# Performance work log

Hardware: AMD Instinct MI355X
Metric: run time of the kernel (lower is better)

## Reference

```python
import jax, jax.numpy as jnp
import numpy as np

N, NX, NQ, NU = 262144, 64, 64, 16
STD = 0.5


def setup_inputs() -> dict:
    key = jax.random.key(0)
    ks = jax.random.split(key, 8)
    x = jax.random.normal(ks[0], (N, NX), jnp.float32)
    u = jax.random.normal(ks[1], (N, NU), jnp.float32)
    A = jax.random.normal(ks[2], (NX, NX), jnp.float32) * STD
    B1 = jax.random.normal(ks[3], (NX, NQ), jnp.float32) * STD
    B2 = jax.random.normal(ks[4], (NX, NU), jnp.float32) * STD
    C1 = jax.random.normal(ks[5], (NQ, NX), jnp.float32) * STD
    # D11 is strictly lower triangular (forward substitution / triangular solve)
    D11 = jnp.tril(jax.random.normal(ks[6], (NQ, NQ), jnp.float32) * STD, -1)
    D12 = jax.random.normal(ks[7], (NQ, NU), jnp.float32) * STD
    bv = jnp.zeros((NQ,), jnp.float32)  # bias=False in original module
    bx = jnp.zeros((NX,), jnp.float32)
    return {"x": x, "u": u, "A": A, "B1": B1, "B2": B2,
            "C1": C1, "D11": D11, "D12": D12, "bv": bv, "bx": bx}


def _calculate_w(x, u, C1, D11, D12, bv):
    """Solve w = act(C1 x + D11 w + D12 u + bv) by forward substitution.
    D11 is strictly lower triangular, so row i of w only depends on rows < i."""
    act = jax.nn.relu
    nq = D11.shape[0]
    base = x @ C1.T + u @ D12.T + bv          # (N, nq): input-dependent part
    eye = jnp.eye(nq, dtype=x.dtype)           # one-hot rows for the scatter

    def step(w, inp):
        d_row, b_col, e = inp                  # (nq,), (N,), (nq,)
        v = b_col + w @ d_row                  # (N,)  uses only already-filled w cols
        w = w + act(v)[:, None] * e            # write column i (matches torch select_w)
        return w, None

    w0 = jnp.zeros((x.shape[0], nq), x.dtype)
    w, _ = jax.lax.scan(step, w0, (D11, base.T, eye))
    return w


def reference(x, u, A, B1, B2, C1, D11, D12, bv, bx):
    # x_dot = A x + B1 w + B2 u + bx
    w = _calculate_w(x, u, C1, D11, D12, bv)
    x_dot = x @ A.T + w @ B1.T + u @ B2.T + bx
    return x_dot
```

## Files before the change

### kernel.cpp

```cpp
#include <hip/hip_runtime.h>
#include <utility>

#define NROWS 262144
#define BT 512
#define RPB 128

typedef float f16v __attribute__((ext_vector_type(16)));


__global__ void prep_kernel(const float* __restrict__ A, const float* __restrict__ B1,
                            const float* __restrict__ B2, const float* __restrict__ C1,
                            const float* __restrict__ D11, const float* __restrict__ D12,
                            const float* __restrict__ bv, const float* __restrict__ bx,
                            float* __restrict__ ws) {
    int g = blockIdx.x * 256 + threadIdx.x;
    if (g < 4096) {
        int r = g >> 6, c = g & 63;
        int to = c * 64 + r;
        ws[0     + to] = C1[g];
        ws[4096  + to] = D11[g];
        ws[9280  + to] = A[g];
        ws[13376 + to] = B1[g];
    }
    if (g < 1024) {
        int r = g >> 4, c = g & 15;
        int to = c * 64 + r;
        ws[8192  + to] = D12[g];
        ws[17472 + to] = B2[g];
    }
    if (g < 64) {
        ws[9216  + g] = bv[g];
        ws[18496 + g] = bx[g];
    }
}

__device__ __forceinline__ f16v lds16(const float* p) { return *(const f16v*)p; }

template<int Q>
__device__ __forceinline__ float qbcast(float v) {
    return __int_as_float(__builtin_amdgcn_update_dpp(
        0, __float_as_int(v), Q * 0x55, 0xF, 0xF, true));
}

template<int I>
__device__ __forceinline__ void substep(f16v& s, const float* D11s, int c16, int c) {
    const float wv = fmaxf(qbcast<(I >> 4)>(s[I & 15]), 0.0f);
    s += lds16(D11s + I * 64 + c16) * wv;
    s[I & 15] = (c == (I >> 4)) ? wv : s[I & 15];
}

template<int... Is>
__device__ __forceinline__ void subst_all(f16v& s, const float* D11s, int c16, int c,
                                          std::integer_sequence<int, Is...>) {
    (substep<Is>(s, D11s, c16, c), ...);
}

template<int J>
__device__ __forceinline__ void b1step(f16v& acc, const f16v& w, const float* B1s, int c16) {
    acc += lds16(B1s + J * 64 + c16) * qbcast<(J >> 4)>(w[J & 15]);
}

template<int... Js>
__device__ __forceinline__ void b1_all(f16v& acc, const f16v& w, const float* B1s, int c16,
                                       std::integer_sequence<int, Js...>) {
    (b1step<Js>(acc, w, B1s, c16), ...);
}

__global__ __launch_bounds__(BT, 4) void renl2_fused(const float* __restrict__ x,
                                                     const float* __restrict__ u,
                                                     const float* __restrict__ ws,
                                                     float* __restrict__ out) {
    __shared__ float sm[9280];
    const int tid = threadIdx.x;
    const int c   = tid & 3;
    const int c16 = c << 4;
    const int r   = tid >> 2;
    const int row = blockIdx.x * RPB + r;

    const float* __restrict__ xr = x + (size_t)row * 64;
    const float* __restrict__ ur = u + (size_t)row * 16;

#pragma unroll 4
    for (int i = tid; i < 9280; i += BT) sm[i] = ws[i];
    __syncthreads();

    f16v s = lds16(sm + 9216 + c16);
#pragma unroll 1
    for (int j = 0; j < 64; j += 4) {
        const float4 xv = *(const float4*)(xr + j);
#pragma unroll
        for (int jj = 0; jj < 4; jj++) {
            const float xs = (jj == 0) ? xv.x : (jj == 1) ? xv.y : (jj == 2) ? xv.z : xv.w;
            s += lds16(sm + (j + jj) * 64 + c16) * xs;
        }
    }
    {
        const float4 uv0 = *(const float4*)(ur);
        const float4 uv1 = *(const float4*)(ur + 4);
        const float4 uv2 = *(const float4*)(ur + 8);
        const float4 uv3 = *(const float4*)(ur + 12);
        const float us[16] = {uv0.x,uv0.y,uv0.z,uv0.w, uv1.x,uv1.y,uv1.z,uv1.w,
                              uv2.x,uv2.y,uv2.z,uv2.w, uv3.x,uv3.y,uv3.z,uv3.w};
#pragma unroll
        for (int j = 0; j < 16; j++)
            s += lds16(sm + 8192 + j * 64 + c16) * us[j];
    }

    subst_all(s, sm + 4096, c16, c, std::make_integer_sequence<int, 64>{});

    __syncthreads();
#pragma unroll 4
    for (int i = tid; i < 9280; i += BT) sm[i] = ws[9280 + i];
    __syncthreads();

    f16v acc = lds16(sm + 9216 + c16);
    b1_all(acc, s, sm + 4096, c16, std::make_integer_sequence<int, 64>{});

#pragma unroll 1
    for (int j = 0; j < 64; j += 4) {
        const float4 xv = *(const float4*)(xr + j);
#pragma unroll
        for (int jj = 0; jj < 4; jj++) {
            const float xs = (jj == 0) ? xv.x : (jj == 1) ? xv.y : (jj == 2) ? xv.z : xv.w;
            acc += lds16(sm + (j + jj) * 64 + c16) * xs;
        }
    }

    {
        const float4 uv0 = *(const float4*)(ur);
        const float4 uv1 = *(const float4*)(ur + 4);
        const float4 uv2 = *(const float4*)(ur + 8);
        const float4 uv3 = *(const float4*)(ur + 12);
        const float us[16] = {uv0.x,uv0.y,uv0.z,uv0.w, uv1.x,uv1.y,uv1.z,uv1.w,
                              uv2.x,uv2.y,uv2.z,uv2.w, uv3.x,uv3.y,uv3.z,uv3.w};
#pragma unroll
        for (int j = 0; j < 16; j++)
            acc += lds16(sm + 8192 + j * 64 + c16) * us[j];
    }

    float* outr = out + (size_t)row * 64;
    *(float4*)(outr + c16)      = float4{acc[0],  acc[1],  acc[2],  acc[3]};
    *(float4*)(outr + c16 + 4)  = float4{acc[4],  acc[5],  acc[6],  acc[7]};
    *(float4*)(outr + c16 + 8)  = float4{acc[8],  acc[9],  acc[10], acc[11]};
    *(float4*)(outr + c16 + 12) = float4{acc[12], acc[13], acc[14], acc[15]};
}

extern "C" void kernel_launch(void* const* d_in, const int* in_sizes, int n_in,
                              void* d_out, int out_size, void* d_ws, size_t ws_size,
                              hipStream_t stream) {
    const float* x   = (const float*)d_in[0];
    const float* u   = (const float*)d_in[1];
    const float* A   = (const float*)d_in[2];
    const float* B1  = (const float*)d_in[3];
    const float* B2  = (const float*)d_in[4];
    const float* C1  = (const float*)d_in[5];
    const float* D11 = (const float*)d_in[6];
    const float* D12 = (const float*)d_in[7];
    const float* bv  = (const float*)d_in[8];
    const float* bx  = (const float*)d_in[9];
    float* out = (float*)d_out;
    float* ws  = (float*)d_ws;

    prep_kernel<<<16, 256, 0, stream>>>(A, B1, B2, C1, D11, D12, bv, bx, ws);
    renl2_fused<<<NROWS / RPB, BT, 0, stream>>>(x, u, ws, out);
}
```

Baseline: 270.0 us.

## Load x/u once into registers, share via DPP, stage all weights in LDS once

```diff
diff --git a/kernel.cpp b/kernel.cpp
--- a/kernel.cpp
+++ b/kernel.cpp
@@ -6,6 +6,7 @@
 #define RPB 128
 
 typedef float f16v __attribute__((ext_vector_type(16)));
+typedef float f4v  __attribute__((ext_vector_type(4)));
 
 
 __global__ void prep_kernel(const float* __restrict__ A, const float* __restrict__ B1,
@@ -56,93 +57,57 @@
 }
 
 template<int J>
-__device__ __forceinline__ void b1step(f16v& acc, const f16v& w, const float* B1s, int c16) {
-    acc += lds16(B1s + J * 64 + c16) * qbcast<(J >> 4)>(w[J & 15]);
+__device__ __forceinline__ void mv64step(f16v& a, const float* Ms, int c16, const f16v& f) {
+    a += lds16(Ms + J * 64 + c16) * qbcast<(J >> 4)>(f[J & 15]);
+}
+template<int... Js>
+__device__ __forceinline__ void mv64(f16v& a, const float* Ms, int c16, const f16v& f,
+                                     std::integer_sequence<int, Js...>) {
+    (mv64step<Js>(a, Ms, c16, f), ...);
 }
 
+template<int J>
+__device__ __forceinline__ void mv16step(f16v& a, const float* Ms, int c16, const f4v& f) {
+    a += lds16(Ms + J * 64 + c16) * qbcast<(J >> 2)>(f[J & 3]);
+}
 template<int... Js>
-__device__ __forceinline__ void b1_all(f16v& acc, const f16v& w, const float* B1s, int c16,
-                                       std::integer_sequence<int, Js...>) {
-    (b1step<Js>(acc, w, B1s, c16), ...);
+__device__ __forceinline__ void mv16(f16v& a, const float* Ms, int c16, const f4v& f,
+                                     std::integer_sequence<int, Js...>) {
+    (mv16step<Js>(a, Ms, c16, f), ...);
 }
 
 __global__ __launch_bounds__(BT, 4) void renl2_fused(const float* __restrict__ x,
                                                      const float* __restrict__ u,
                                                      const float* __restrict__ ws,
                                                      float* __restrict__ out) {
-    __shared__ float sm[9280];
+    __shared__ __align__(64) float sm[18560];
     const int tid = threadIdx.x;
     const int c   = tid & 3;
     const int c16 = c << 4;
-    const int r   = tid >> 2;
-    const int row = blockIdx.x * RPB + r;
+    const size_t row0 = (size_t)blockIdx.x * RPB;
 
-    const float* __restrict__ xr = x + (size_t)row * 64;
-    const float* __restrict__ ur = u + (size_t)row * 16;
+    const f16v xf = *(const f16v*)(x + row0 * 64 + (size_t)tid * 16);
+    const f4v  uf = *(const f4v*) (u + row0 * 16 + (size_t)tid * 4);
 
-#pragma unroll 4
-    for (int i = tid; i < 9280; i += BT) sm[i] = ws[i];
+    const float4* wsv = (const float4*)ws;
+    float4* smv = (float4*)sm;
+#pragma unroll
+    for (int i = 0; i < 9; i++) smv[tid + i * BT] = wsv[tid + i * BT];
+    if (tid < 4640 - 9 * BT) smv[tid + 9 * BT] = wsv[tid + 9 * BT];
     __syncthreads();
 
     f16v s = lds16(sm + 9216 + c16);
-#pragma unroll 1
-    for (int j = 0; j < 64; j += 4) {
-        const float4 xv = *(const float4*)(xr + j);
-#pragma unroll
-        for (int jj = 0; jj < 4; jj++) {
-            const float xs = (jj == 0) ? xv.x : (jj == 1) ? xv.y : (jj == 2) ? xv.z : xv.w;
-            s += lds16(sm + (j + jj) * 64 + c16) * xs;
-        }
-    }
-    {
-        const float4 uv0 = *(const float4*)(ur);
-        const float4 uv1 = *(const float4*)(ur + 4);
-        const float4 uv2 = *(const float4*)(ur + 8);
-        const float4 uv3 = *(const float4*)(ur + 12);
-        const float us[16] = {uv0.x,uv0.y,uv0.z,uv0.w, uv1.x,uv1.y,uv1.z,uv1.w,
-                              uv2.x,uv2.y,uv2.z,uv2.w, uv3.x,uv3.y,uv3.z,uv3.w};
-#pragma unroll
-        for (int j = 0; j < 16; j++)
-            s += lds16(sm + 8192 + j * 64 + c16) * us[j];
-    }
+    mv64(s, sm + 0,    c16, xf, std::make_integer_sequence<int, 64>{});
+    mv16(s, sm + 8192, c16, uf, std::make_integer_sequence<int, 16>{});
 
     subst_all(s, sm + 4096, c16, c, std::make_integer_sequence<int, 64>{});
 
-    __syncthreads();
-#pragma unroll 4
-    for (int i = tid; i < 9280; i += BT) sm[i] = ws[9280 + i];
-    __syncthreads();
+    f16v acc = lds16(sm + 18496 + c16);
+    mv64(acc, sm + 13376, c16, s,  std::make_integer_sequence<int, 64>{});
+    mv64(acc, sm + 9280,  c16, xf, std::make_integer_sequence<int, 64>{});
+    mv16(acc, sm + 17472, c16, uf, std::make_integer_sequence<int, 16>{});
 
-    f16v acc = lds16(sm + 9216 + c16);
-    b1_all(acc, s, sm + 4096, c16, std::make_integer_sequence<int, 64>{});
-
-#pragma unroll 1
-    for (int j = 0; j < 64; j += 4) {
-        const float4 xv = *(const float4*)(xr + j);
-#pragma unroll
-        for (int jj = 0; jj < 4; jj++) {
-            const float xs = (jj == 0) ? xv.x : (jj == 1) ? xv.y : (jj == 2) ? xv.z : xv.w;
-            acc += lds16(sm + (j + jj) * 64 + c16) * xs;
-        }
-    }
-
-    {
-        const float4 uv0 = *(const float4*)(ur);
-        const float4 uv1 = *(const float4*)(ur + 4);
-        const float4 uv2 = *(const float4*)(ur + 8);
-        const float4 uv3 = *(const float4*)(ur + 12);
-        const float us[16] = {uv0.x,uv0.y,uv0.z,uv0.w, uv1.x,uv1.y,uv1.z,uv1.w,
-                              uv2.x,uv2.y,uv2.z,uv2.w, uv3.x,uv3.y,uv3.z,uv3.w};
-#pragma unroll
-        for (int j = 0; j < 16; j++)
-            acc += lds16(sm + 8192 + j * 64 + c16) * us[j];
-    }
-
-    float* outr = out + (size_t)row * 64;
-    *(float4*)(outr + c16)      = float4{acc[0],  acc[1],  acc[2],  acc[3]};
-    *(float4*)(outr + c16 + 4)  = float4{acc[4],  acc[5],  acc[6],  acc[7]};
-    *(float4*)(outr + c16 + 8)  = float4{acc[8],  acc[9],  acc[10], acc[11]};
-    *(float4*)(outr + c16 + 12) = float4{acc[12], acc[13], acc[14], acc[15]};
+    *(f16v*)(out + (row0 + (size_t)(tid >> 2)) * 64 + c16) = acc;
 }
 
 extern "C" void kernel_launch(void* const* d_in, const int* in_sizes, int n_in,
```

Result: slower. 330.7 us (+22.5%).
